# Kernel optimization log

Measured on AMD Instinct MI355X. Metric: run time of the kernel, lower is better.

The kernel has to match this reference:

```python
import jax, jax.numpy as jnp
import numpy as np

B = 256        # graphs per batch (python loop in original, vectorized here)
N = 512        # nodes per graph
DEG = 16       # avg degree
E_PER = N * DEG
T = 64         # num_node_types
D = 128        # gnn_hidden_dim


def setup_inputs() -> dict:
    key = jax.random.key(0)
    ks = jax.random.split(key, 8)
    node_feat = jax.random.randint(ks[0], (B * N,), 0, T)
    offs = (jnp.arange(B) * N)[:, None]
    src = (jax.random.randint(ks[1], (B, E_PER), 0, N) + offs).reshape(-1)
    dst = (jax.random.randint(ks[2], (B, E_PER), 0, N) + offs).reshape(-1)
    emb_table = jax.random.normal(ks[3], (T, D), dtype=jnp.float32) * 0.02
    W1 = jax.random.normal(ks[4], (D, D), dtype=jnp.float32) * (1.0 / np.sqrt(D))
    b1 = jnp.zeros((D,), dtype=jnp.float32)
    W2 = jax.random.normal(ks[5], (D, D), dtype=jnp.float32) * (1.0 / np.sqrt(D))
    b2 = jnp.zeros((D,), dtype=jnp.float32)
    return {"node_feat": node_feat, "src": src, "dst": dst,
            "emb_table": emb_table, "W1": W1, "b1": b1, "W2": W2, "b2": b2}


def _gcn_layer(h, src, dst, out_isqrt, in_isqrt, W, b, n):
    # DGL GraphConv, norm='both': D_in^{-1/2} A D_out^{-1/2} h W + b
    m = (h * out_isqrt[:, None])[src]                      # [E, D] gather
    agg = jax.ops.segment_sum(m, dst, num_segments=n)      # [Ntot, D] scatter
    return (agg * in_isqrt[:, None]) @ W + b


def reference(node_feat, src, dst, emb_table, W1, b1, W2, b2):
    n = node_feat.shape[0]
    ones = jnp.ones(src.shape[0], dtype=emb_table.dtype)
    deg_out = jnp.clip(jax.ops.segment_sum(ones, src, num_segments=n), 1.0)
    deg_in = jnp.clip(jax.ops.segment_sum(ones, dst, num_segments=n), 1.0)
    out_isqrt = jax.lax.rsqrt(deg_out)
    in_isqrt = jax.lax.rsqrt(deg_in)

    h = emb_table[node_feat]                                # [Ntot, D]
    # layer 1 (dropout is eval-mode identity) + relu, layer 2 + relu
    h = jax.nn.relu(_gcn_layer(h, src, dst, out_isqrt, in_isqrt, W1, b1, n))
    h = jax.nn.relu(_gcn_layer(h, src, dst, out_isqrt, in_isqrt, W2, b2, n))

    # dgl.mean_nodes per graph, then mean_gnn_embeddings + stack -> [B, D]
    gid = jnp.arange(n) // N
    hg = jax.ops.segment_sum(h, gid, num_segments=B) / float(N)
    return hg
```

## Files before the change

kernel.cpp:

```cpp
#include <hip/hip_runtime.h>
#include <stdint.h>

#define GRAPHS 256
#define NPG    512
#define EPG    8192
#define NTOT   (GRAPHS*NPG)

typedef __attribute__((ext_vector_type(8))) short s16x8;
typedef __attribute__((ext_vector_type(4))) float f32x4;

__device__ __forceinline__ float bf2f(unsigned short u){
  union { unsigned int i; float f; } c; c.i = ((unsigned int)u)<<16; return c.f;
}
__device__ __forceinline__ unsigned short f2bf(float f){
  union { float f; unsigned int i; } c; c.f = f;
  unsigned int r = c.i + 0x7fffu + ((c.i>>16)&1u);
  return (unsigned short)(r>>16);
}

__global__ __launch_bounds__(512) void k_csr(const int* __restrict__ src,
      const int* __restrict__ dst, const int* __restrict__ ntype,
      const float* __restrict__ emb, const float* __restrict__ W1,
      const float* __restrict__ W2,
      unsigned int* __restrict__ sorted_g, int* __restrict__ start_g,
      float* __restrict__ out_isqrt, unsigned short* __restrict__ EW1T,
      unsigned short* __restrict__ W2T){
  __shared__ int hist[NPG], cursor[NPG], co[NPG], cs[NPG+1];
  __shared__ unsigned short ntype_sh[NPG];
  __shared__ unsigned int sorted[EPG];
  const int tid=threadIdx.x;
  if (blockIdx.x >= GRAPHS){
    const int gid = (blockIdx.x-GRAPHS)*512 + tid;
    if (gid < 8192){
      const int t = gid>>7, c = gid&127;
      float acc=0.f;
      #pragma unroll 4
      for (int k=0;k<128;k++) acc += emb[t*128+k]*W1[k*128+c];
      EW1T[c*64+t]=f2bf(acc);
    } else {
      const int i = gid - 8192;
      const int k = i>>7, n = i&127;
      W2T[n*128+k] = f2bf(W2[k*128+n]);
    }
    return;
  }
  const int b=blockIdx.x, eb=b*EPG, nb=b*NPG;
  hist[tid]=0; co[tid]=0; ntype_sh[tid]=(unsigned short)ntype[nb+tid];
  __syncthreads();
  int4 d4[4], s4[4];
  {
    const int4* dv = (const int4*)(dst+eb);
    const int4* sv = (const int4*)(src+eb);
    #pragma unroll
    for (int j=0;j<4;j++){
      d4[j]=dv[tid + j*512];
      s4[j]=sv[tid + j*512];
      atomicAdd(&hist[d4[j].x&(NPG-1)],1); atomicAdd(&hist[d4[j].y&(NPG-1)],1);
      atomicAdd(&hist[d4[j].z&(NPG-1)],1); atomicAdd(&hist[d4[j].w&(NPG-1)],1);
      atomicAdd(&co[s4[j].x&(NPG-1)],1);   atomicAdd(&co[s4[j].y&(NPG-1)],1);
      atomicAdd(&co[s4[j].z&(NPG-1)],1);   atomicAdd(&co[s4[j].w&(NPG-1)],1);
    }
  }
  __syncthreads();
  if (tid<64){
    int carry=0;
    #pragma unroll
    for (int c=0;c<8;c++){
      int sc=hist[64*c+tid];
      #pragma unroll
      for (int off=1;off<64;off<<=1){ int y=__shfl_up(sc,off); if (tid>=off) sc+=y; }
      cs[64*c+tid+1]=carry+sc;
      carry+=__shfl(sc,63);
    }
    if (tid==0) cs[0]=0;
  }
  __syncthreads();
  cursor[tid]=cs[tid];
  __syncthreads();
  #pragma unroll
  for (int j=0;j<4;j++){
    int dl, s, pos;
    dl=d4[j].x&(NPG-1); s=s4[j].x&(NPG-1);
    pos=atomicAdd(&cursor[dl],1);
    sorted[pos]=((unsigned int)dl<<15)|((unsigned int)ntype_sh[s]<<9)|(unsigned int)s;
    dl=d4[j].y&(NPG-1); s=s4[j].y&(NPG-1);
    pos=atomicAdd(&cursor[dl],1);
    sorted[pos]=((unsigned int)dl<<15)|((unsigned int)ntype_sh[s]<<9)|(unsigned int)s;
    dl=d4[j].z&(NPG-1); s=s4[j].z&(NPG-1);
    pos=atomicAdd(&cursor[dl],1);
    sorted[pos]=((unsigned int)dl<<15)|((unsigned int)ntype_sh[s]<<9)|(unsigned int)s;
    dl=d4[j].w&(NPG-1); s=s4[j].w&(NPG-1);
    pos=atomicAdd(&cursor[dl],1);
    sorted[pos]=((unsigned int)dl<<15)|((unsigned int)ntype_sh[s]<<9)|(unsigned int)s;
  }
  __syncthreads();
  for (int i=tid;i<EPG;i+=512) sorted_g[(size_t)eb+i] = sorted[i];
  if (tid==0) start_g[b*(NPG+1)+NPG]=cs[NPG];
  start_g[b*(NPG+1)+tid]=cs[tid];
  {
    int a=co[tid]; if(a<1)a=1;
    out_isqrt[nb+tid]=rsqrtf((float)a);
  }
}

#define A1_LDS 75280
__global__ __launch_bounds__(512) void k_agg1(
      const unsigned int* __restrict__ sorted_g, const int* __restrict__ start_g,
      const unsigned short* __restrict__ EW1T, const float* __restrict__ out_isqrt,
      const float* __restrict__ b1, unsigned short* __restrict__ h1F){
  extern __shared__ char smem[];
  int*   Sint   = (int*)(smem);
  float* wsc    = (float*)(smem + 69632);
  int*   wint   = (int*)  (smem + 71680);
  int*   sstart = (int*)  (smem + 73728);
  float* bsh    = (float*)(smem + 74756);
  const int bid=blockIdx.x;
  const int b    = ((bid>>4)<<3) | (bid&7);
  const int half = (bid>>3)&1;
  const int v0=half*256, nb=b*NPG, tid=threadIdx.x;
  for (int i=tid; i<(256*68)/4; i+=512) ((f32x4*)Sint)[i]=(f32x4){0.f,0.f,0.f,0.f};
  for (int i=tid; i<NPG; i+=512){
    const float w = out_isqrt[nb+i];
    wsc[i]=w;
    wint[i]=(int)(w*1048576.f);
  }
  for (int i=tid; i<257; i+=512) sstart[i]=start_g[b*(NPG+1)+v0+i];
  if (tid<128) bsh[tid]=b1[tid];
  __syncthreads();
  {
    const int beg=sstart[0], end=sstart[256];
    const unsigned int* sg = sorted_g + (size_t)b*EPG;
    for (int i=beg+tid; i<end; i+=512){
      const unsigned int ent = sg[i];
      const int dl = (int)(ent>>15) - v0;
      const int t  = (ent>>9)&63;
      atomicAdd(&Sint[dl*68 + t], wint[ent&511]);
    }
  }
  __syncthreads();
  const int wave=tid>>6, lane=tid&63, l16=lane&15, quad=lane>>4;
  f32x4 acc[2][8];
  #pragma unroll
  for (int rt=0;rt<2;rt++)
    #pragma unroll
    for (int nt=0;nt<8;nt++) acc[rt][nt]=(f32x4){0.f,0.f,0.f,0.f};
  #pragma unroll
  for (int ks=0; ks<4; ++ks){
    const int kc = (ks&1)*32 + quad*8;
    s16x8 a[2];
    #pragma unroll
    for (int rt=0;rt<2;rt++){
      const int m = (wave*2+rt)*16 + l16;
      const int* sp = &Sint[m*68 + kc];
      union { s16x8 v; unsigned short u[8]; } pk;
      #pragma unroll
      for (int j=0;j<8;j++){
        const float f = (float)sp[j] * (1.f/1048576.f);
        const unsigned short hi = f2bf(f);
        pk.u[j] = (ks<2) ? hi : f2bf(f - bf2f(hi));
      }
      a[rt]=pk.v;
    }
    #pragma unroll
    for (int nt=0;nt<8;nt++){
      s16x8 bfr=__builtin_bit_cast(s16x8,
          *(const uint4*)(EW1T + (size_t)(nt*16+l16)*64 + kc));
      #pragma unroll
      for (int rt=0;rt<2;rt++)
        acc[rt][nt]=__builtin_amdgcn_mfma_f32_16x16x32_bf16(a[rt],bfr,acc[rt][nt],0,0,0);
    }
  }
  #pragma unroll
  for (int rt=0;rt<2;rt++){
    const int W = wave*2+rt;
    const int mloc = W*16 + quad*4;
    float isq[4], os[4];
    #pragma unroll
    for (int r=0;r<4;r++){
      int d = sstart[mloc+r+1]-sstart[mloc+r]; if (d<1) d=1;
      isq[r]=rsqrtf((float)d);
      os[r]=wsc[v0+mloc+r];
    }
    const int ks2 = half*8 + (W>>1);
    const int q2  = ((W&1)<<1) | (quad>>1);
    const int j0  = (quad&1)*4;
    #pragma unroll
    for (int nt=0;nt<8;nt++){
      const int col = nt*16+l16;
      const float bb = bsh[col];
      ushort4 st;
      float v;
      v = fmaxf(acc[rt][nt][0]*isq[0]+bb,0.f)*os[0]; st.x=f2bf(v);
      v = fmaxf(acc[rt][nt][1]*isq[1]+bb,0.f)*os[1]; st.y=f2bf(v);
      v = fmaxf(acc[rt][nt][2]*isq[2]+bb,0.f)*os[2]; st.z=f2bf(v);
      v = fmaxf(acc[rt][nt][3]*isq[3]+bb,0.f)*os[3]; st.w=f2bf(v);
      const size_t off = ((((size_t)b*16 + ks2)*8 + nt)*64 + q2*16 + l16)*8 + j0;
      *(ushort4*)(h1F + off) = st;
    }
  }
}

#define A2_LDS 67080
__global__ __launch_bounds__(512) void k_agg2(
      const unsigned int* __restrict__ sorted_g, const int* __restrict__ start_g,
      const unsigned short* __restrict__ h1F, unsigned short* __restrict__ M1F){
  extern __shared__ char smem[];
  unsigned char* A = (unsigned char*)smem;
  unsigned int* A32 = (unsigned int*)smem;
  int* sstart = (int*)(smem + 66560);
  const int bid=blockIdx.x;
  const int b  = ((bid>>5)<<3) | (bid&7);
  const int dt = (bid>>3)&3;
  const int v0=dt*128, tid=threadIdx.x;
  for (int i=tid; i<66560/16; i+=512) ((uint4*)smem)[i]=(uint4){0u,0u,0u,0u};
  for (int i=tid; i<129; i+=512) sstart[i]=start_g[b*(NPG+1)+v0+i];
  __syncthreads();
  {
    const int beg=sstart[0], end=sstart[128];
    const unsigned int* sg = sorted_g + (size_t)b*EPG;
    for (int i=beg+tid; i<end; i+=512){
      const unsigned int ent = sg[i];
      const int dl = (int)(ent>>15) - v0;
      const int s  = ent&511;
      atomicAdd(&A32[dl*130 + (s>>2)], 1u<<((s&3)*8));
    }
  }
  __syncthreads();
  const int wave=tid>>6, lane=tid&63, l16=lane&15, quad=lane>>4;
  const int mg=wave>>1, ng=wave&1;
  f32x4 acc[2][4];
  #pragma unroll
  for (int rt=0;rt<2;rt++)
    #pragma unroll
    for (int ct=0;ct<4;ct++) acc[rt][ct]=(f32x4){0.f,0.f,0.f,0.f};
  const uint4* bp[4];
  #pragma unroll
  for (int ct=0;ct<4;ct++)
    bp[ct] = (const uint4*)h1F + (((size_t)b*16)*8 + (ng*4+ct))*64 + lane;
  const unsigned char* Ab[2];
  #pragma unroll
  for (int rt=0;rt<2;rt++)
    Ab[rt] = A + ((mg*2+rt)*16 + l16)*520 + quad*8;
  #pragma unroll 2
  for (int ks=0; ks<16; ++ks){
    uint4 bq[4];
    #pragma unroll
    for (int ct=0;ct<4;ct++) bq[ct] = bp[ct][(size_t)ks*512];
    s16x8 afr[2];
    #pragma unroll
    for (int rt=0;rt<2;rt++){
      const uint2 aw = *(const uint2*)(Ab[rt] + ks*32);
      union { s16x8 v; unsigned short u[8]; } pk;
      #pragma unroll
      for (int j=0;j<4;j++){
        const float f0 = (float)((aw.x>>(8*j))&0xffu);
        const float f1 = (float)((aw.y>>(8*j))&0xffu);
        pk.u[j]   = (unsigned short)(__builtin_bit_cast(unsigned int, f0)>>16);
        pk.u[j+4] = (unsigned short)(__builtin_bit_cast(unsigned int, f1)>>16);
      }
      afr[rt]=pk.v;
    }
    #pragma unroll
    for (int rt=0;rt<2;rt++)
      #pragma unroll
      for (int ct=0;ct<4;ct++)
        acc[rt][ct]=__builtin_amdgcn_mfma_f32_16x16x32_bf16(afr[rt],
            __builtin_bit_cast(s16x8, bq[ct]), acc[rt][ct],0,0,0);
  }
  #pragma unroll
  for (int rt=0;rt<2;rt++){
    const int mloc=(mg*2+rt)*16 + quad*4;
    const int M = dt*8 + mg*2 + rt;
    float isq[4];
    #pragma unroll
    for (int r=0;r<4;r++){
      int d=sstart[mloc+r+1]-sstart[mloc+r]; if (d<1) d=1;
      isq[r]=rsqrtf((float)d);
    }
    #pragma unroll
    for (int ct=0;ct<4;ct++){
      const int ks2   = ng*2 + (ct>>1);
      const int quad2 = ((ct&1)<<1) | (l16>>3);
      const int j     = l16&7;
      unsigned short* base = M1F
          + ((((size_t)b*32+M)*4+ks2)*64 + quad2*16)*8 + j;
      #pragma unroll
      for (int r=0;r<4;r++)
        base[(size_t)(quad*4+r)*8] = f2bf(acc[rt][ct][r]*isq[r]);
    }
  }
}

__global__ __launch_bounds__(512) void k_gemm2(const unsigned short* __restrict__ M1F,
      const unsigned short* __restrict__ W2T, const float* __restrict__ b2,
      float* __restrict__ out){
  __shared__ __align__(16) unsigned short WT[128][136];
  __shared__ float bsh[128];
  __shared__ float colpart[8][128];
  const int b=blockIdx.x, tid=threadIdx.x;
  for (int idx=tid; idx<2048; idx+=512){
    const int row = idx>>4, c8 = idx&15;
    *(uint4*)&WT[row][c8*8] = *(const uint4*)(W2T + row*128 + c8*8);
  }
  if (tid<128) bsh[tid]=b2[tid];
  __syncthreads();
  const int wave=tid>>6, lane=tid&63, l16=lane&15, quad=lane>>4;
  float p[8];
  #pragma unroll
  for (int i=0;i<8;i++) p[i]=0.f;
  for (int chunk=0; chunk<2; ++chunk){
    f32x4 acc[2][8];
    #pragma unroll
    for (int rt=0;rt<2;rt++)
      #pragma unroll
      for (int ct=0;ct<8;ct++) acc[rt][ct]=(f32x4){0.f,0.f,0.f,0.f};
    #pragma unroll
    for (int ks=0;ks<4;ks++){
      s16x8 a[2], bf[8];
      #pragma unroll
      for (int rt=0;rt<2;rt++){
        const int M = wave*4 + chunk*2 + rt;
        a[rt]=__builtin_bit_cast(s16x8, *(const uint4*)(M1F
            + ((((size_t)b*32+M)*4+ks)*64 + lane)*8));
      }
      #pragma unroll
      for (int ct=0;ct<8;ct++)
        bf[ct]=__builtin_bit_cast(s16x8, *(const uint4*)&WT[ct*16+l16][ks*32+quad*8]);
      #pragma unroll
      for (int rt=0;rt<2;rt++)
        #pragma unroll
        for (int ct=0;ct<8;ct++)
          acc[rt][ct]=__builtin_amdgcn_mfma_f32_16x16x32_bf16(a[rt],bf[ct],acc[rt][ct],0,0,0);
    }
    #pragma unroll
    for (int rt=0;rt<2;rt++)
      #pragma unroll
      for (int ct=0;ct<8;ct++)
        #pragma unroll
        for (int r=0;r<4;r++){
          const int col=ct*16+l16;
          p[ct] += fmaxf(acc[rt][ct][r]+bsh[col],0.f);
        }
  }
  #pragma unroll
  for (int ct=0;ct<8;ct++){
    p[ct] += __shfl_xor(p[ct],16);
    p[ct] += __shfl_xor(p[ct],32);
  }
  if (quad==0){
    #pragma unroll
    for (int ct=0;ct<8;ct++) colpart[wave][ct*16+l16]=p[ct];
  }
  __syncthreads();
  if (tid<128){
    float s=0.f;
    #pragma unroll
    for (int w=0;w<8;w++) s+=colpart[w][tid];
    out[b*128+tid]=s*(1.f/512.f);
  }
}

extern "C" void kernel_launch(void* const* d_in, const int* in_sizes, int n_in,
                              void* d_out, int out_size, void* d_ws, size_t ws_size,
                              hipStream_t stream){
  const int* node_feat = (const int*)d_in[0];
  const int* src = (const int*)d_in[1];
  const int* dst = (const int*)d_in[2];
  const float* emb = (const float*)d_in[3];
  const float* W1  = (const float*)d_in[4];
  const float* b1  = (const float*)d_in[5];
  const float* W2  = (const float*)d_in[6];
  const float* b2  = (const float*)d_in[7];

  char* ws = (char*)d_ws;
  float* out_isqrt        = (float*)(ws);
  int* start_g            = (int*)(ws + 524288);
  unsigned int* sorted_g  = (unsigned int*)(ws + 1049600);
  unsigned short* EW1T    = (unsigned short*)(ws + 9438208);
  unsigned short* W2T     = (unsigned short*)(ws + 9454592);
  unsigned short* h1F     = (unsigned short*)(ws + 9487360);
  unsigned short* M1F     = (unsigned short*)(ws + 43041792);

  (void)hipFuncSetAttribute(reinterpret_cast<const void*>(&k_agg1),
        hipFuncAttributeMaxDynamicSharedMemorySize, A1_LDS);
  (void)hipFuncSetAttribute(reinterpret_cast<const void*>(&k_agg2),
        hipFuncAttributeMaxDynamicSharedMemorySize, A2_LDS);

  k_csr<<<GRAPHS+48,512,0,stream>>>(src,dst,node_feat,emb,W1,W2,
        sorted_g,start_g,out_isqrt,EW1T,W2T);
  k_agg1<<<GRAPHS*2,512,A1_LDS,stream>>>(sorted_g,start_g,EW1T,out_isqrt,b1,h1F);
  k_agg2<<<GRAPHS*4,512,A2_LDS,stream>>>(sorted_g,start_g,h1F,M1F);
  k_gemm2<<<GRAPHS,512,0,stream>>>(M1F,W2T,b2,(float*)d_out);
}
```

Measured before the change: 148.5 us.

## Apply W2 before layer-2 aggregation and fuse pooling into aggregation kernel

Uses associativity, A(hW) = (Ah)W, to run the layer-2 weight GEMM inside k_agg1 on the layer-1 output staged in LDS. k_agg2 then aggregates the pre-multiplied features and applies bias, ReLU and per-graph partial mean pooling directly, so the M1F intermediate and the separate k_gemm2 kernel go away. A small k_final kernel sums the four partials per graph. This trades an extra GEMM stage and LDS round trip in k_agg1 for fewer global passes and one less heavy launch. It also adds one more bf16 rounding at a different point, which slightly changes numerics.

Result: faster. 143.5 us (-3.4%).

```diff
diff --git a/kernel.cpp b/kernel.cpp
--- a/kernel.cpp
+++ b/kernel.cpp
@@ -24,7 +24,7 @@
       const float* __restrict__ W2,
       unsigned int* __restrict__ sorted_g, int* __restrict__ start_g,
       float* __restrict__ out_isqrt, unsigned short* __restrict__ EW1T,
-      unsigned short* __restrict__ W2T){
+      unsigned short* __restrict__ W2F){
   __shared__ int hist[NPG], cursor[NPG], co[NPG], cs[NPG+1];
   __shared__ unsigned short ntype_sh[NPG];
   __shared__ unsigned int sorted[EPG];
@@ -39,8 +39,10 @@
       EW1T[c*64+t]=f2bf(acc);
     } else {
       const int i = gid - 8192;
-      const int k = i>>7, n = i&127;
-      W2T[n*128+k] = f2bf(W2[k*128+n]);
+      const int ks = i>>12, nt=(i>>9)&7, lane=(i>>3)&63, j=i&7;
+      const int k = ks*32 + (lane>>4)*8 + j;
+      const int n = nt*16 + (lane&15);
+      W2F[i] = f2bf(W2[k*128+n]);
     }
     return;
   }
@@ -107,9 +109,11 @@
 __global__ __launch_bounds__(512) void k_agg1(
       const unsigned int* __restrict__ sorted_g, const int* __restrict__ start_g,
       const unsigned short* __restrict__ EW1T, const float* __restrict__ out_isqrt,
-      const float* __restrict__ b1, unsigned short* __restrict__ h1F){
+      const float* __restrict__ b1, const unsigned short* __restrict__ W2F,
+      unsigned short* __restrict__ H2F){
   extern __shared__ char smem[];
   int*   Sint   = (int*)(smem);
+  unsigned short* h1sh = (unsigned short*)(smem);
   float* wsc    = (float*)(smem + 69632);
   int*   wint   = (int*)  (smem + 71680);
   int*   sstart = (int*)  (smem + 73728);
@@ -170,50 +174,91 @@
         acc[rt][nt]=__builtin_amdgcn_mfma_f32_16x16x32_bf16(a[rt],bfr,acc[rt][nt],0,0,0);
     }
   }
+  float isq[2][4], os[2][4];
+  #pragma unroll
+  for (int rt=0;rt<2;rt++){
+    const int mloc = (wave*2+rt)*16 + quad*4;
+    #pragma unroll
+    for (int r=0;r<4;r++){
+      int d = sstart[mloc+r+1]-sstart[mloc+r]; if (d<1) d=1;
+      isq[rt][r]=rsqrtf((float)d);
+      os[rt][r]=wsc[v0+mloc+r];
+    }
+  }
+  __syncthreads();
+  #pragma unroll
+  for (int rt=0;rt<2;rt++){
+    const int mloc = (wave*2+rt)*16 + quad*4;
+    #pragma unroll
+    for (int nt=0;nt<8;nt++){
+      const int col = nt*16+l16;
+      const float bb = bsh[col];
+      #pragma unroll
+      for (int r=0;r<4;r++){
+        const float v = fmaxf(acc[rt][nt][r]*isq[rt][r]+bb,0.f)*os[rt][r];
+        h1sh[(mloc+r)*136 + col] = f2bf(v);
+      }
+    }
+  }
+  __syncthreads();
+  f32x4 acc2[2][8];
+  #pragma unroll
+  for (int rt=0;rt<2;rt++)
+    #pragma unroll
+    for (int nt=0;nt<8;nt++) acc2[rt][nt]=(f32x4){0.f,0.f,0.f,0.f};
+  #pragma unroll
+  for (int ks=0; ks<4; ++ks){
+    s16x8 a2[2];
+    #pragma unroll
+    for (int rt=0;rt<2;rt++){
+      const int m = (wave*2+rt)*16 + l16;
+      a2[rt]=__builtin_bit_cast(s16x8,
+          *(const uint4*)(h1sh + m*136 + ks*32 + quad*8));
+    }
+    #pragma unroll
+    for (int nt=0;nt<8;nt++){
+      s16x8 bfr=__builtin_bit_cast(s16x8,
+          *(const uint4*)(W2F + (size_t)(((ks*8+nt)*64)+lane)*8));
+      #pragma unroll
+      for (int rt=0;rt<2;rt++)
+        acc2[rt][nt]=__builtin_amdgcn_mfma_f32_16x16x32_bf16(a2[rt],bfr,acc2[rt][nt],0,0,0);
+    }
+  }
   #pragma unroll
   for (int rt=0;rt<2;rt++){
     const int W = wave*2+rt;
-    const int mloc = W*16 + quad*4;
-    float isq[4], os[4];
-    #pragma unroll
-    for (int r=0;r<4;r++){
-      int d = sstart[mloc+r+1]-sstart[mloc+r]; if (d<1) d=1;
-      isq[r]=rsqrtf((float)d);
-      os[r]=wsc[v0+mloc+r];
-    }
     const int ks2 = half*8 + (W>>1);
     const int q2  = ((W&1)<<1) | (quad>>1);
     const int j0  = (quad&1)*4;
     #pragma unroll
     for (int nt=0;nt<8;nt++){
-      const int col = nt*16+l16;
-      const float bb = bsh[col];
       ushort4 st;
-      float v;
-      v = fmaxf(acc[rt][nt][0]*isq[0]+bb,0.f)*os[0]; st.x=f2bf(v);
-      v = fmaxf(acc[rt][nt][1]*isq[1]+bb,0.f)*os[1]; st.y=f2bf(v);
-      v = fmaxf(acc[rt][nt][2]*isq[2]+bb,0.f)*os[2]; st.z=f2bf(v);
-      v = fmaxf(acc[rt][nt][3]*isq[3]+bb,0.f)*os[3]; st.w=f2bf(v);
+      st.x=f2bf(acc2[rt][nt][0]); st.y=f2bf(acc2[rt][nt][1]);
+      st.z=f2bf(acc2[rt][nt][2]); st.w=f2bf(acc2[rt][nt][3]);
       const size_t off = ((((size_t)b*16 + ks2)*8 + nt)*64 + q2*16 + l16)*8 + j0;
-      *(ushort4*)(h1F + off) = st;
-    }
-  }
-}
-
-#define A2_LDS 67080
+      *(ushort4*)(H2F + off) = st;
+    }
+  }
+}
+
+#define A2_LDS 67592
 __global__ __launch_bounds__(512) void k_agg2(
       const unsigned int* __restrict__ sorted_g, const int* __restrict__ start_g,
-      const unsigned short* __restrict__ h1F, unsigned short* __restrict__ M1F){
+      const unsigned short* __restrict__ H2F, const float* __restrict__ b2,
+      float* __restrict__ partial){
   extern __shared__ char smem[];
   unsigned char* A = (unsigned char*)smem;
   unsigned int* A32 = (unsigned int*)smem;
+  float* red = (float*)smem;
   int* sstart = (int*)(smem + 66560);
+  float* bsh  = (float*)(smem + 67080);
   const int bid=blockIdx.x;
   const int b  = ((bid>>5)<<3) | (bid&7);
   const int dt = (bid>>3)&3;
   const int v0=dt*128, tid=threadIdx.x;
   for (int i=tid; i<66560/16; i+=512) ((uint4*)smem)[i]=(uint4){0u,0u,0u,0u};
   for (int i=tid; i<129; i+=512) sstart[i]=start_g[b*(NPG+1)+v0+i];
+  if (tid<128) bsh[tid]=b2[tid];
   __syncthreads();
   {
     const int beg=sstart[0], end=sstart[128];
@@ -236,7 +281,7 @@
   const uint4* bp[4];
   #pragma unroll
   for (int ct=0;ct<4;ct++)
-    bp[ct] = (const uint4*)h1F + (((size_t)b*16)*8 + (ng*4+ct))*64 + lane;
+    bp[ct] = (const uint4*)H2F + (((size_t)b*16)*8 + (ng*4+ct))*64 + lane;
   const unsigned char* Ab[2];
   #pragma unroll
   for (int rt=0;rt<2;rt++)
@@ -267,10 +312,12 @@
         acc[rt][ct]=__builtin_amdgcn_mfma_f32_16x16x32_bf16(afr[rt],
             __builtin_bit_cast(s16x8, bq[ct]), acc[rt][ct],0,0,0);
   }
+  float p[4];
+  #pragma unroll
+  for (int ct=0;ct<4;ct++) p[ct]=0.f;
   #pragma unroll
   for (int rt=0;rt<2;rt++){
     const int mloc=(mg*2+rt)*16 + quad*4;
-    const int M = dt*8 + mg*2 + rt;
     float isq[4];
     #pragma unroll
     for (int r=0;r<4;r++){
@@ -279,85 +326,39 @@
     }
     #pragma unroll
     for (int ct=0;ct<4;ct++){
-      const int ks2   = ng*2 + (ct>>1);
-      const int quad2 = ((ct&1)<<1) | (l16>>3);
-      const int j     = l16&7;
-      unsigned short* base = M1F
-          + ((((size_t)b*32+M)*4+ks2)*64 + quad2*16)*8 + j;
+      const int col=ng*64 + ct*16 + l16;
+      const float bb = bsh[col];
       #pragma unroll
       for (int r=0;r<4;r++)
-        base[(size_t)(quad*4+r)*8] = f2bf(acc[rt][ct][r]*isq[r]);
-    }
-  }
-}
-
-__global__ __launch_bounds__(512) void k_gemm2(const unsigned short* __restrict__ M1F,
-      const unsigned short* __restrict__ W2T, const float* __restrict__ b2,
-      float* __restrict__ out){
-  __shared__ __align__(16) unsigned short WT[128][136];
-  __shared__ float bsh[128];
-  __shared__ float colpart[8][128];
-  const int b=blockIdx.x, tid=threadIdx.x;
-  for (int idx=tid; idx<2048; idx+=512){
-    const int row = idx>>4, c8 = idx&15;
-    *(uint4*)&WT[row][c8*8] = *(const uint4*)(W2T + row*128 + c8*8);
-  }
-  if (tid<128) bsh[tid]=b2[tid];
-  __syncthreads();
-  const int wave=tid>>6, lane=tid&63, l16=lane&15, quad=lane>>4;
-  float p[8];
-  #pragma unroll
-  for (int i=0;i<8;i++) p[i]=0.f;
-  for (int chunk=0; chunk<2; ++chunk){
-    f32x4 acc[2][8];
-    #pragma unroll
-    for (int rt=0;rt<2;rt++)
-      #pragma unroll
-      for (int ct=0;ct<8;ct++) acc[rt][ct]=(f32x4){0.f,0.f,0.f,0.f};
-    #pragma unroll
-    for (int ks=0;ks<4;ks++){
-      s16x8 a[2], bf[8];
-      #pragma unroll
-      for (int rt=0;rt<2;rt++){
-        const int M = wave*4 + chunk*2 + rt;
-        a[rt]=__builtin_bit_cast(s16x8, *(const uint4*)(M1F
-            + ((((size_t)b*32+M)*4+ks)*64 + lane)*8));
-      }
-      #pragma unroll
-      for (int ct=0;ct<8;ct++)
-        bf[ct]=__builtin_bit_cast(s16x8, *(const uint4*)&WT[ct*16+l16][ks*32+quad*8]);
-      #pragma unroll
-      for (int rt=0;rt<2;rt++)
-        #pragma unroll
-        for (int ct=0;ct<8;ct++)
-          acc[rt][ct]=__builtin_amdgcn_mfma_f32_16x16x32_bf16(a[rt],bf[ct],acc[rt][ct],0,0,0);
-    }
-    #pragma unroll
-    for (int rt=0;rt<2;rt++)
-      #pragma unroll
-      for (int ct=0;ct<8;ct++)
-        #pragma unroll
-        for (int r=0;r<4;r++){
-          const int col=ct*16+l16;
-          p[ct] += fmaxf(acc[rt][ct][r]+bsh[col],0.f);
-        }
-  }
-  #pragma unroll
-  for (int ct=0;ct<8;ct++){
+        p[ct] += fmaxf(acc[rt][ct][r]*isq[r]+bb,0.f);
+    }
+  }
+  #pragma unroll
+  for (int ct=0;ct<4;ct++){
     p[ct] += __shfl_xor(p[ct],16);
     p[ct] += __shfl_xor(p[ct],32);
   }
+  __syncthreads();
   if (quad==0){
     #pragma unroll
-    for (int ct=0;ct<8;ct++) colpart[wave][ct*16+l16]=p[ct];
+    for (int ct=0;ct<4;ct++) red[wave*64 + ct*16+l16]=p[ct];
   }
   __syncthreads();
   if (tid<128){
+    const int col=tid, cg=col>>6, c6=col&63;
     float s=0.f;
     #pragma unroll
-    for (int w=0;w<8;w++) s+=colpart[w][tid];
-    out[b*128+tid]=s*(1.f/512.f);
-  }
+    for (int m2=0;m2<4;m2++) s += red[(m2*2+cg)*64 + c6];
+    partial[(size_t)(b*4+dt)*128 + col]=s;
+  }
+}
+
+__global__ __launch_bounds__(256) void k_final(const float* __restrict__ partial,
+      float* __restrict__ out){
+  const int gid = blockIdx.x*256 + threadIdx.x;
+  const int b=gid>>7, c=gid&127;
+  const float* p = partial + (size_t)(b*4)*128 + c;
+  out[gid] = (p[0]+p[128]+p[256]+p[384])*(1.f/512.f);
 }
 
 extern "C" void kernel_launch(void* const* d_in, const int* in_sizes, int n_in,
@@ -377,9 +378,9 @@
   int* start_g            = (int*)(ws + 524288);
   unsigned int* sorted_g  = (unsigned int*)(ws + 1049600);
   unsigned short* EW1T    = (unsigned short*)(ws + 9438208);
-  unsigned short* W2T     = (unsigned short*)(ws + 9454592);
-  unsigned short* h1F     = (unsigned short*)(ws + 9487360);
-  unsigned short* M1F     = (unsigned short*)(ws + 43041792);
+  unsigned short* W2F     = (unsigned short*)(ws + 9454592);
+  unsigned short* H2F     = (unsigned short*)(ws + 9487360);
+  float* partial          = (float*)(ws + 43041792);
 
   (void)hipFuncSetAttribute(reinterpret_cast<const void*>(&k_agg1),
         hipFuncAttributeMaxDynamicSharedMemorySize, A1_LDS);
@@ -387,8 +388,9 @@
         hipFuncAttributeMaxDynamicSharedMemorySize, A2_LDS);
 
   k_csr<<<GRAPHS+48,512,0,stream>>>(src,dst,node_feat,emb,W1,W2,
-        sorted_g,start_g,out_isqrt,EW1T,W2T);
-  k_agg1<<<GRAPHS*2,512,A1_LDS,stream>>>(sorted_g,start_g,EW1T,out_isqrt,b1,h1F);
-  k_agg2<<<GRAPHS*4,512,A2_LDS,stream>>>(sorted_g,start_g,h1F,M1F);
-  k_gemm2<<<GRAPHS,512,0,stream>>>(M1F,W2T,b2,(float*)d_out);
-}
+        sorted_g,start_g,out_isqrt,EW1T,W2F);
+  k_agg1<<<GRAPHS*2,512,A1_LDS,stream>>>(sorted_g,start_g,EW1T,out_isqrt,b1,
+        W2F,H2F);
+  k_agg2<<<GRAPHS*4,512,A2_LDS,stream>>>(sorted_g,start_g,H2F,b2,partial);
+  k_final<<<128,256,0,stream>>>(partial,(float*)d_out);
+}
```
